# Performance work log

Measured on AMD Instinct MI355X. Metric: run time of the kernel, lower is better.

The kernel has to match this reference:

```python
import jax, jax.numpy as jnp
import numpy as np

B, S, E, H = 4, 2048, 1024, 16
DH = E // H  # head_dim = 64


def setup_inputs() -> dict:
    key = jax.random.key(0)
    k1, k2, k3 = jax.random.split(key, 3)
    x = jax.random.normal(k1, (B, S, E), dtype=jnp.float32)
    # xavier-uniform-like scale for dense kernels
    Wqkv = jax.random.normal(k2, (E, 3 * E), dtype=jnp.float32) * (1.0 / np.sqrt(E))
    Wout = jax.random.normal(k3, (E, E), dtype=jnp.float32) * (1.0 / np.sqrt(E))
    return {"x": x, "Wqkv": Wqkv, "Wout": Wout}


def reference(x, Wqkv, Wout):
    b, s, e = x.shape
    qkv = jnp.einsum("bse,ef->bsf", x, Wqkv)            # [B,S,3E]
    qkv = qkv.reshape(b, s, H, 3 * DH).transpose(0, 2, 1, 3)  # [B,H,S,3*DH]
    q, k, v = jnp.split(qkv, 3, axis=-1)                # each [B,H,S,DH]
    scale = 1.0 / jnp.sqrt(jnp.asarray(DH, dtype=x.dtype))
    scores = jnp.einsum("bhqd,bhkd->bhqk", q, k) * scale  # [B,H,S,S] materialized
    attn = jax.nn.softmax(scores, axis=-1)
    values = jnp.einsum("bhqk,bhkd->bhqd", attn, v)     # [B,H,S,DH]
    values = values.transpose(0, 2, 1, 3).reshape(b, s, e)
    out = jnp.einsum("bse,ef->bsf", values, Wout)       # [B,S,E]
    return out
```

## Files before the change

kernel.cpp:

```cpp
#include <hip/hip_runtime.h>

typedef __attribute__((ext_vector_type(8))) __bf16 bf16x8;
typedef __attribute__((ext_vector_type(4))) float f32x4;

#define LOG2E 1.4426950408889634f
#define QSCALE (0.125f * LOG2E)

static __device__ __forceinline__ void gl_lds16(const void* g, void* l) {
  __builtin_amdgcn_global_load_lds(
      (__attribute__((address_space(1))) void*)(g),
      (__attribute__((address_space(3))) void*)(l), 16, 0, 0);
}

__global__ __launch_bounds__(256) void convert_f32_bf16(const float* __restrict__ in,
                                                        __bf16* __restrict__ out,
                                                        int n8) {
  const int i = blockIdx.x * 256 + threadIdx.x;
  if (i >= n8) return;
  const f32x4 a = *(const f32x4*)(in + (size_t)i * 8);
  const f32x4 b = *(const f32x4*)(in + (size_t)i * 8 + 4);
  bf16x8 o;
#pragma unroll
  for (int j = 0; j < 4; ++j) o[j] = (__bf16)a[j];
#pragma unroll
  for (int j = 0; j < 4; ++j) o[4 + j] = (__bf16)b[j];
  *(bf16x8*)(out + (size_t)i * 8) = o;
}

__global__ __launch_bounds__(256) void transpose_f32_bf16(
    const float* __restrict__ in, __bf16* __restrict__ out, int R, int C) {
  __shared__ __bf16 tile[64][72];
  const int t = threadIdx.x;
  const int c0 = blockIdx.x * 64;
  const int r0 = blockIdx.y * 64;
  const int lr = t >> 2;
  const int lc = (t & 3) * 16;
  const float* src = in + (size_t)(r0 + lr) * C + c0 + lc;
  bf16x8 w0, w1;
#pragma unroll
  for (int j = 0; j < 2; ++j) {
    const f32x4 a = *(const f32x4*)(src + j * 8);
    const f32x4 b = *(const f32x4*)(src + j * 8 + 4);
    bf16x8 o;
#pragma unroll
    for (int k = 0; k < 4; ++k) o[k] = (__bf16)a[k];
#pragma unroll
    for (int k = 0; k < 4; ++k) o[4 + k] = (__bf16)b[k];
    *(bf16x8*)&tile[lr][lc + j * 8] = o;
  }
  __syncthreads();
#pragma unroll
  for (int j = 0; j < 8; ++j) {
    w0[j] = tile[lc + j][lr];
    w1[j] = tile[lc + 8 + j][lr];
  }
  __bf16* dst = out + (size_t)(c0 + lr) * R + r0 + lc;
  *(bf16x8*)dst = w0;
  *(bf16x8*)(dst + 8) = w1;
}


#define STAGE_A(TT, KH)                                                  \
  do {                                                                   \
    char* d_ = lds + ((TT) & 1) * 16384 + (KH) * 8192 + t * 16;          \
    gl_lds16(Ab + gsrc + (TT) * 64 + (KH) * 32, d_);                     \
  } while (0)

#define STAGE_B(TT, KH)                                                  \
  do {                                                                   \
    char* d_ = lds + 32768 + ((TT) & 1) * 16384 + (KH) * 8192 + t * 16;  \
    gl_lds16(Bb + gsrc + (TT) * 64 + (KH) * 32, d_);                     \
  } while (0)

#define READ_AB(KK)                                                              \
  do {                                                                           \
    const char* pa_ = lds + buf * 16384 + (KK) * 8192 + wm * 4096 + lfo;         \
    a0 = *(const bf16x8*)pa_;                                                    \
    a1 = *(const bf16x8*)(pa_ + 1024);                                           \
    a2 = *(const bf16x8*)(pa_ + 2048);                                           \
    a3 = *(const bf16x8*)(pa_ + 3072);                                           \
    const char* pb_ = lds + 32768 + buf * 16384 + (KK) * 8192 + wn * 2048 + lfo; \
    b0 = *(const bf16x8*)pb_;                                                    \
    b1 = *(const bf16x8*)(pb_ + 1024);                                           \
  } while (0)

#define MROW(MI, AV)                                                             \
  acc[MI][0] = __builtin_amdgcn_mfma_f32_16x16x32_bf16(AV, b0, acc[MI][0], 0, 0, 0); \
  acc[MI][1] = __builtin_amdgcn_mfma_f32_16x16x32_bf16(AV, b1, acc[MI][1], 0, 0, 0);

#define MFMA8()                        \
  do {                                 \
    __builtin_amdgcn_s_setprio(1);     \
    MROW(0, a0)                        \
    MROW(1, a1)                        \
    MROW(2, a2)                        \
    MROW(3, a3)                        \
    __builtin_amdgcn_s_setprio(0);     \
  } while (0)

template <int EPI>
__global__ __launch_bounds__(512, 4) void gemm128(
    const __bf16* __restrict__ A, const __bf16* __restrict__ Bt,
    float* __restrict__ Cf, __bf16* __restrict__ q_ws, __bf16* __restrict__ k_ws,
    __bf16* __restrict__ vT_ws, int M, int N, int K) {
  (void)M;
  extern __shared__ char lds[];
  const int t = threadIdx.x;
  const int lane = t & 63;
  const int quad = lane >> 4, l15 = lane & 15;
  const int w = t >> 6;
  const int wm = w >> 2, wn = w & 3;

  const int olid = blockIdx.y * gridDim.x + blockIdx.x;
  const int xcd = olid & 7, loc = olid >> 3;
  const int m0 = (xcd * 8 + (loc & 7)) * 128;
  const int n0 = (loc >> 3) * 128;

  const int LB = t * 16;
  const int r_in = (LB >> 6) & 15;
  const int ch = ((LB >> 5) & 1) ^ ((r_in >> 3) & 1);
  const int rowS = (LB >> 10) * 16 + r_in;
  const int kcS = ch * 16 + ((LB >> 4) & 1) * 8;
  const __bf16* Ab = A + (size_t)m0 * K;
  const __bf16* Bb = Bt + (size_t)n0 * K;
  const size_t gsrc = (size_t)rowS * K + kcS;

  const int lfo = l15 * 64 + ((((quad >> 1) ^ (l15 >> 3)) & 1) << 5) + ((quad & 1) << 4);

  const f32x4 fzero = {0.f, 0.f, 0.f, 0.f};
  f32x4 acc[4][2];
#pragma unroll
  for (int i = 0; i < 4; ++i) {
    acc[i][0] = fzero;
    acc[i][1] = fzero;
  }

  const int nt = K >> 6;
  bf16x8 a0, a1, a2, a3, b0, b1;

  STAGE_A(0, 0);
  STAGE_B(0, 0);
  STAGE_A(0, 1);
  STAGE_B(0, 1);
  if (nt > 1) {
    STAGE_A(1, 0);
    STAGE_B(1, 0);
    asm volatile("s_waitcnt vmcnt(4)");
  } else {
    asm volatile("s_waitcnt vmcnt(0)");
  }
  __builtin_amdgcn_s_barrier();

  for (int tt = 0; tt < nt; ++tt) {
    const int buf = tt & 1;
    READ_AB(0);
    if (tt + 1 < nt) {
      STAGE_A(tt + 1, 1);
      STAGE_B(tt + 1, 1);
    }
    __builtin_amdgcn_s_barrier();
    asm volatile("s_waitcnt lgkmcnt(0)");
    MFMA8();
    if (tt + 1 < nt)
      asm volatile("s_waitcnt vmcnt(4)");
    else
      asm volatile("s_waitcnt vmcnt(0)");
    __builtin_amdgcn_s_barrier();
    READ_AB(1);
    if (tt + 2 < nt) {
      STAGE_A(tt + 2, 0);
      STAGE_B(tt + 2, 0);
    }
    __builtin_amdgcn_s_barrier();
    asm volatile("s_waitcnt lgkmcnt(0)");
    MFMA8();
    if (tt + 2 < nt)
      asm volatile("s_waitcnt vmcnt(4)");
    else if (tt + 1 < nt)
      asm volatile("s_waitcnt vmcnt(2)");
    else
      asm volatile("s_waitcnt vmcnt(0)");
    __builtin_amdgcn_s_barrier();
  }

#pragma unroll
  for (int mi = 0; mi < 4; ++mi) {
#pragma unroll
    for (int r = 0; r < 4; ++r) {
      const int row = m0 + wm * 64 + mi * 16 + quad * 4 + r;
#pragma unroll
      for (int ni = 0; ni < 2; ++ni) {
        const int col = n0 + wn * 32 + ni * 16 + l15;
        const float v = acc[mi][ni][r];
        if (EPI == 0) {
          const int b = row >> 11, s = row & 2047;
          const int h = col / 192;
          const int rr = col - h * 192;
          const int ty = rr >> 6, d = rr & 63;
          const int bh = b * 16 + h;
          if (ty == 0)
            q_ws[((size_t)bh * 2048 + s) * 64 + d] = (__bf16)(v * QSCALE);
          else if (ty == 1)
            k_ws[((size_t)bh * 2048 + s) * 64 + d] = (__bf16)v;
          else
            vT_ws[((size_t)bh * 64 + d) * 2048 + s] = (__bf16)v;
        } else {
          Cf[(size_t)row * N + col] = v;
        }
      }
    }
  }
}

__global__ __launch_bounds__(256) void flash_attn(
    const __bf16* __restrict__ q_ws, const __bf16* __restrict__ k_ws,
    const __bf16* __restrict__ vT_ws, __bf16* __restrict__ values, int bh0) {
  __shared__ __bf16 sK[64][72];
  __shared__ __bf16 sVt[64][72];
  __shared__ __bf16 sP[4][32][68];
  const int t = threadIdx.x;
  const int lane = t & 63, w = t >> 6, quad = lane >> 4, l15 = lane & 15;
  const int qt = blockIdx.x;
  const int bh = blockIdx.y + bh0;
  const __bf16* Qb = q_ws + (size_t)bh * 2048 * 64;
  const __bf16* Kb = k_ws + (size_t)bh * 2048 * 64;
  const __bf16* Vtb = vT_ws + (size_t)bh * 64 * 2048;
  const int qrow0 = qt * 128 + w * 32;

  bf16x8 qf[2][2];
#pragma unroll
  for (int mi = 0; mi < 2; ++mi)
#pragma unroll
    for (int ks = 0; ks < 2; ++ks)
      qf[mi][ks] = *(const bf16x8*)(Qb + (size_t)(qrow0 + mi * 16 + l15) * 64 +
                                    ks * 32 + quad * 8);

  bf16x8 ones;
#pragma unroll
  for (int j = 0; j < 8; ++j) ones[j] = (__bf16)1.0f;

  const f32x4 fzero = {0.f, 0.f, 0.f, 0.f};
  f32x4 accO[2][4];
  f32x4 accL[2];
#pragma unroll
  for (int mi = 0; mi < 2; ++mi) {
    accL[mi] = fzero;
#pragma unroll
    for (int ni = 0; ni < 4; ++ni) accO[mi][ni] = fzero;
  }

  const int srow = t >> 2;
  const int scol = (t & 3) * 16;

  bf16x8 ka, kb2, va, vb;
  {
    const __bf16* ks0 = Kb + (size_t)srow * 64 + scol;
    ka = *(const bf16x8*)ks0;
    kb2 = *(const bf16x8*)(ks0 + 8);
    const __bf16* vs0 = Vtb + (size_t)srow * 2048 + scol;
    va = *(const bf16x8*)vs0;
    vb = *(const bf16x8*)(vs0 + 8);
  }

  for (int kt = 0; kt < 32; ++kt) {
    *(bf16x8*)&sK[srow][scol] = ka;
    *(bf16x8*)&sK[srow][scol + 8] = kb2;
    *(bf16x8*)&sVt[srow][scol] = va;
    *(bf16x8*)&sVt[srow][scol + 8] = vb;
    __syncthreads();

    if (kt < 31) {
      const __bf16* ksn = Kb + (size_t)((kt + 1) * 64 + srow) * 64 + scol;
      ka = *(const bf16x8*)ksn;
      kb2 = *(const bf16x8*)(ksn + 8);
      const __bf16* vsn = Vtb + (size_t)srow * 2048 + (kt + 1) * 64 + scol;
      va = *(const bf16x8*)vsn;
      vb = *(const bf16x8*)(vsn + 8);
    }

    f32x4 accS[2][4];
#pragma unroll
    for (int mi = 0; mi < 2; ++mi)
#pragma unroll
      for (int ni = 0; ni < 4; ++ni) accS[mi][ni] = fzero;
#pragma unroll
    for (int ks = 0; ks < 2; ++ks) {
      bf16x8 kf[4];
#pragma unroll
      for (int ni = 0; ni < 4; ++ni)
        kf[ni] = *(const bf16x8*)&sK[ni * 16 + l15][ks * 32 + quad * 8];
#pragma unroll
      for (int mi = 0; mi < 2; ++mi)
#pragma unroll
        for (int ni = 0; ni < 4; ++ni)
          accS[mi][ni] = __builtin_amdgcn_mfma_f32_16x16x32_bf16(
              qf[mi][ks], kf[ni], accS[mi][ni], 0, 0, 0);
    }

#pragma unroll
    for (int mi = 0; mi < 2; ++mi) {
#pragma unroll
      for (int r = 0; r < 4; ++r) {
        const int prow = mi * 16 + quad * 4 + r;
#pragma unroll
        for (int ni = 0; ni < 4; ++ni) {
          const float p = __builtin_amdgcn_exp2f(accS[mi][ni][r]);
          sP[w][prow][ni * 16 + l15] = (__bf16)p;
        }
      }
    }
    __threadfence_block();

#pragma unroll
    for (int ks = 0; ks < 2; ++ks) {
      bf16x8 vf[4], pf[2];
#pragma unroll
      for (int ni = 0; ni < 4; ++ni)
        vf[ni] = *(const bf16x8*)&sVt[ni * 16 + l15][ks * 32 + quad * 8];
#pragma unroll
      for (int mi = 0; mi < 2; ++mi)
        pf[mi] = *(const bf16x8*)&sP[w][mi * 16 + l15][ks * 32 + quad * 8];
#pragma unroll
      for (int mi = 0; mi < 2; ++mi) {
#pragma unroll
        for (int ni = 0; ni < 4; ++ni)
          accO[mi][ni] = __builtin_amdgcn_mfma_f32_16x16x32_bf16(
              pf[mi], vf[ni], accO[mi][ni], 0, 0, 0);
        accL[mi] = __builtin_amdgcn_mfma_f32_16x16x32_bf16(pf[mi], ones, accL[mi],
                                                           0, 0, 0);
      }
    }
    __syncthreads();
  }

  const int b = bh >> 4, h = bh & 15;
#pragma unroll
  for (int mi = 0; mi < 2; ++mi) {
#pragma unroll
    for (int r = 0; r < 4; ++r) {
      const float inv = 1.0f / accL[mi][r];
      const int s = qrow0 + mi * 16 + quad * 4 + r;
#pragma unroll
      for (int ni = 0; ni < 4; ++ni)
        values[((size_t)(b * 2048 + s)) * 1024 + h * 64 + ni * 16 + l15] =
            (__bf16)(accO[mi][ni][r] * inv);
    }
  }
}

extern "C" void kernel_launch(void* const* d_in, const int* in_sizes, int n_in,
                              void* d_out, int out_size, void* d_ws, size_t ws_size,
                              hipStream_t stream) {
  (void)out_size; (void)ws_size;
  float* out = (float*)d_out;
  char* wsb = (char*)d_ws;
  __bf16* xb = (__bf16*)(wsb + 256);
  __bf16* WqkvT = xb + 8388608;
  __bf16* WoutT = WqkvT + 3145728;
  __bf16* q_ws = WoutT + 1048576;
  __bf16* k_ws = q_ws + 8388608;
  __bf16* vT_ws = k_ws + 8388608;
  __bf16* values = xb;

  const float *px = (const float*)d_in[0], *pw = (const float*)d_in[1],
              *po = (const float*)d_in[2];
  for (int i = 0; i < n_in; ++i) {
    if (in_sizes[i] == 8388608) px = (const float*)d_in[i];
    else if (in_sizes[i] == 3145728) pw = (const float*)d_in[i];
    else if (in_sizes[i] == 1048576) po = (const float*)d_in[i];
  }

  hipFuncSetAttribute(reinterpret_cast<const void*>(&gemm128<0>),
                      hipFuncAttributeMaxDynamicSharedMemorySize, 65536);
  hipFuncSetAttribute(reinterpret_cast<const void*>(&gemm128<1>),
                      hipFuncAttributeMaxDynamicSharedMemorySize, 65536);

  convert_f32_bf16<<<4096, 256, 0, stream>>>(px, xb, 1048576);
  transpose_f32_bf16<<<dim3(48, 16), 256, 0, stream>>>(pw, WqkvT, 1024, 3072);
  transpose_f32_bf16<<<dim3(16, 16), 256, 0, stream>>>(po, WoutT, 1024, 1024);
  gemm128<0><<<dim3(64, 24), 512, 65536, stream>>>(xb, WqkvT, nullptr, q_ws, k_ws,
                                                   vT_ws, 8192, 3072, 1024);
  flash_attn<<<dim3(16, 32), 256, 0, stream>>>(q_ws, k_ws, vT_ws, values, 0);
  flash_attn<<<dim3(16, 32), 256, 0, stream>>>(q_ws, k_ws, vT_ws, values, 32);
  gemm128<1><<<dim3(64, 8), 512, 65536, stream>>>(values, WoutT, out, nullptr,
                                                  nullptr, nullptr, 8192, 1024, 1024);
}
```

Before: 308.3 us.

## Use 4-wave GEMM blocks with 64x64 warp tiles and merge launches

The GEMM kernel changes from 8 waves per block with 64x32 warp tiles to 4 waves with 64x64 warp tiles, so each thread issues two LDS staging loads per k-half and each wave runs 16 MFMAs per k-step. The aim is more register-level reuse of A fragments and fewer LDS reads per MFMA. The cost is higher register pressure and less latency hiding per block. The two weight-transpose launches are merged into one kernel, and the two flash-attention launches into one grid, to cut launch overhead.

```diff
diff --git a/kernel.cpp b/kernel.cpp
--- a/kernel.cpp
+++ b/kernel.cpp
@@ -27,11 +27,21 @@
   *(bf16x8*)(out + (size_t)i * 8) = o;
 }
 
-__global__ __launch_bounds__(256) void transpose_f32_bf16(
-    const float* __restrict__ in, __bf16* __restrict__ out, int R, int C) {
+__global__ __launch_bounds__(256) void transpose_weights(
+    const float* __restrict__ Wqkv, const float* __restrict__ Wout,
+    __bf16* __restrict__ WqkvT, __bf16* __restrict__ WoutT) {
   __shared__ __bf16 tile[64][72];
+  const int bx = blockIdx.x;
+  const float* in;
+  __bf16* out;
+  int C, c0;
+  if (bx < 48) {
+    in = Wqkv; out = WqkvT; C = 3072; c0 = bx * 64;
+  } else {
+    in = Wout; out = WoutT; C = 1024; c0 = (bx - 48) * 64;
+  }
+  const int R = 1024;
   const int t = threadIdx.x;
-  const int c0 = blockIdx.x * 64;
   const int r0 = blockIdx.y * 64;
   const int lr = t >> 2;
   const int lc = (t & 3) * 16;
@@ -62,14 +72,18 @@
 
 #define STAGE_A(TT, KH)                                                  \
   do {                                                                   \
+    const size_t kg_ = (TT) * 64 + (KH) * 32;                            \
     char* d_ = lds + ((TT) & 1) * 16384 + (KH) * 8192 + t * 16;          \
-    gl_lds16(Ab + gsrc + (TT) * 64 + (KH) * 32, d_);                     \
+    gl_lds16(Ab + g0 + kg_, d_);                                         \
+    gl_lds16(Ab + g1 + kg_, d_ + 4096);                                  \
   } while (0)
 
 #define STAGE_B(TT, KH)                                                  \
   do {                                                                   \
+    const size_t kg_ = (TT) * 64 + (KH) * 32;                            \
     char* d_ = lds + 32768 + ((TT) & 1) * 16384 + (KH) * 8192 + t * 16;  \
-    gl_lds16(Bb + gsrc + (TT) * 64 + (KH) * 32, d_);                     \
+    gl_lds16(Bb + g0 + kg_, d_);                                         \
+    gl_lds16(Bb + g1 + kg_, d_ + 4096);                                  \
   } while (0)
 
 #define READ_AB(KK)                                                              \
@@ -79,16 +93,20 @@
     a1 = *(const bf16x8*)(pa_ + 1024);                                           \
     a2 = *(const bf16x8*)(pa_ + 2048);                                           \
     a3 = *(const bf16x8*)(pa_ + 3072);                                           \
-    const char* pb_ = lds + 32768 + buf * 16384 + (KK) * 8192 + wn * 2048 + lfo; \
+    const char* pb_ = lds + 32768 + buf * 16384 + (KK) * 8192 + wn * 4096 + lfo; \
     b0 = *(const bf16x8*)pb_;                                                    \
     b1 = *(const bf16x8*)(pb_ + 1024);                                           \
+    b2 = *(const bf16x8*)(pb_ + 2048);                                           \
+    b3 = *(const bf16x8*)(pb_ + 3072);                                           \
   } while (0)
 
-#define MROW(MI, AV)                                                             \
+#define MROW(MI, AV)                                                                 \
   acc[MI][0] = __builtin_amdgcn_mfma_f32_16x16x32_bf16(AV, b0, acc[MI][0], 0, 0, 0); \
-  acc[MI][1] = __builtin_amdgcn_mfma_f32_16x16x32_bf16(AV, b1, acc[MI][1], 0, 0, 0);
-
-#define MFMA8()                        \
+  acc[MI][1] = __builtin_amdgcn_mfma_f32_16x16x32_bf16(AV, b1, acc[MI][1], 0, 0, 0); \
+  acc[MI][2] = __builtin_amdgcn_mfma_f32_16x16x32_bf16(AV, b2, acc[MI][2], 0, 0, 0); \
+  acc[MI][3] = __builtin_amdgcn_mfma_f32_16x16x32_bf16(AV, b3, acc[MI][3], 0, 0, 0);
+
+#define MFMA16()                       \
   do {                                 \
     __builtin_amdgcn_s_setprio(1);     \
     MROW(0, a0)                        \
@@ -99,7 +117,7 @@
   } while (0)
 
 template <int EPI>
-__global__ __launch_bounds__(512, 4) void gemm128(
+__global__ __launch_bounds__(256, 2) void gemm128(
     const __bf16* __restrict__ A, const __bf16* __restrict__ Bt,
     float* __restrict__ Cf, __bf16* __restrict__ q_ws, __bf16* __restrict__ k_ws,
     __bf16* __restrict__ vT_ws, int M, int N, int K) {
@@ -109,34 +127,38 @@
   const int lane = t & 63;
   const int quad = lane >> 4, l15 = lane & 15;
   const int w = t >> 6;
-  const int wm = w >> 2, wn = w & 3;
+  const int wm = w >> 1, wn = w & 1;
 
   const int olid = blockIdx.y * gridDim.x + blockIdx.x;
   const int xcd = olid & 7, loc = olid >> 3;
   const int m0 = (xcd * 8 + (loc & 7)) * 128;
   const int n0 = (loc >> 3) * 128;
 
-  const int LB = t * 16;
-  const int r_in = (LB >> 6) & 15;
-  const int ch = ((LB >> 5) & 1) ^ ((r_in >> 3) & 1);
-  const int rowS = (LB >> 10) * 16 + r_in;
-  const int kcS = ch * 16 + ((LB >> 4) & 1) * 8;
+  int rowS[2], kcS[2];
+#pragma unroll
+  for (int l = 0; l < 2; ++l) {
+    const int LB = l * 4096 + t * 16;
+    const int r_in = (LB >> 6) & 15;
+    const int ch = ((LB >> 5) & 1) ^ ((r_in >> 3) & 1);
+    rowS[l] = (LB >> 10) * 16 + r_in;
+    kcS[l] = ch * 16 + ((LB >> 4) & 1) * 8;
+  }
   const __bf16* Ab = A + (size_t)m0 * K;
   const __bf16* Bb = Bt + (size_t)n0 * K;
-  const size_t gsrc = (size_t)rowS * K + kcS;
+  const size_t g0 = (size_t)rowS[0] * K + kcS[0];
+  const size_t g1 = (size_t)rowS[1] * K + kcS[1];
 
   const int lfo = l15 * 64 + ((((quad >> 1) ^ (l15 >> 3)) & 1) << 5) + ((quad & 1) << 4);
 
   const f32x4 fzero = {0.f, 0.f, 0.f, 0.f};
-  f32x4 acc[4][2];
-#pragma unroll
-  for (int i = 0; i < 4; ++i) {
-    acc[i][0] = fzero;
-    acc[i][1] = fzero;
-  }
+  f32x4 acc[4][4];
+#pragma unroll
+  for (int i = 0; i < 4; ++i)
+#pragma unroll
+    for (int j = 0; j < 4; ++j) acc[i][j] = fzero;
 
   const int nt = K >> 6;
-  bf16x8 a0, a1, a2, a3, b0, b1;
+  bf16x8 a0, a1, a2, a3, b0, b1, b2, b3;
 
   STAGE_A(0, 0);
   STAGE_B(0, 0);
@@ -160,9 +182,9 @@
     }
     __builtin_amdgcn_s_barrier();
     asm volatile("s_waitcnt lgkmcnt(0)");
-    MFMA8();
+    MFMA16();
     if (tt + 1 < nt)
-      asm volatile("s_waitcnt vmcnt(4)");
+      asm volatile("s_waitcnt vmcnt(8)");
     else
       asm volatile("s_waitcnt vmcnt(0)");
     __builtin_amdgcn_s_barrier();
@@ -173,11 +195,11 @@
     }
     __builtin_amdgcn_s_barrier();
     asm volatile("s_waitcnt lgkmcnt(0)");
-    MFMA8();
+    MFMA16();
     if (tt + 2 < nt)
+      asm volatile("s_waitcnt vmcnt(8)");
+    else if (tt + 1 < nt)
       asm volatile("s_waitcnt vmcnt(4)");
-    else if (tt + 1 < nt)
-      asm volatile("s_waitcnt vmcnt(2)");
     else
       asm volatile("s_waitcnt vmcnt(0)");
     __builtin_amdgcn_s_barrier();
@@ -189,8 +211,8 @@
     for (int r = 0; r < 4; ++r) {
       const int row = m0 + wm * 64 + mi * 16 + quad * 4 + r;
 #pragma unroll
-      for (int ni = 0; ni < 2; ++ni) {
-        const int col = n0 + wn * 32 + ni * 16 + l15;
+      for (int ni = 0; ni < 4; ++ni) {
+        const int col = n0 + wn * 64 + ni * 16 + l15;
         const float v = acc[mi][ni][r];
         if (EPI == 0) {
           const int b = row >> 11, s = row & 2047;
@@ -214,14 +236,14 @@
 
 __global__ __launch_bounds__(256) void flash_attn(
     const __bf16* __restrict__ q_ws, const __bf16* __restrict__ k_ws,
-    const __bf16* __restrict__ vT_ws, __bf16* __restrict__ values, int bh0) {
+    const __bf16* __restrict__ vT_ws, __bf16* __restrict__ values) {
   __shared__ __bf16 sK[64][72];
   __shared__ __bf16 sVt[64][72];
   __shared__ __bf16 sP[4][32][68];
   const int t = threadIdx.x;
   const int lane = t & 63, w = t >> 6, quad = lane >> 4, l15 = lane & 15;
   const int qt = blockIdx.x;
-  const int bh = blockIdx.y + bh0;
+  const int bh = blockIdx.y;
   const __bf16* Qb = q_ws + (size_t)bh * 2048 * 64;
   const __bf16* Kb = k_ws + (size_t)bh * 2048 * 64;
   const __bf16* Vtb = vT_ws + (size_t)bh * 64 * 2048;
@@ -376,12 +398,10 @@
                       hipFuncAttributeMaxDynamicSharedMemorySize, 65536);
 
   convert_f32_bf16<<<4096, 256, 0, stream>>>(px, xb, 1048576);
-  transpose_f32_bf16<<<dim3(48, 16), 256, 0, stream>>>(pw, WqkvT, 1024, 3072);
-  transpose_f32_bf16<<<dim3(16, 16), 256, 0, stream>>>(po, WoutT, 1024, 1024);
-  gemm128<0><<<dim3(64, 24), 512, 65536, stream>>>(xb, WqkvT, nullptr, q_ws, k_ws,
+  transpose_weights<<<dim3(64, 16), 256, 0, stream>>>(pw, po, WqkvT, WoutT);
+  gemm128<0><<<dim3(64, 24), 256, 65536, stream>>>(xb, WqkvT, nullptr, q_ws, k_ws,
                                                    vT_ws, 8192, 3072, 1024);
-  flash_attn<<<dim3(16, 32), 256, 0, stream>>>(q_ws, k_ws, vT_ws, values, 0);
-  flash_attn<<<dim3(16, 32), 256, 0, stream>>>(q_ws, k_ws, vT_ws, values, 32);
-  gemm128<1><<<dim3(64, 8), 512, 65536, stream>>>(values, WoutT, out, nullptr,
+  flash_attn<<<dim3(16, 64), 256, 0, stream>>>(q_ws, k_ws, vT_ws, values);
+  gemm128<1><<<dim3(64, 8), 256, 65536, stream>>>(values, WoutT, out, nullptr,
                                                   nullptr, nullptr, 8192, 1024, 1024);
 }
```

New measurement: 310.0 us. Within noise of the previous version (+0.5%).
